# Kernel optimization log

Measured on AMD Instinct MI355X. Metric: run time of the kernel, lower is better.

## Reference

```python
import jax, jax.numpy as jnp
import numpy as np

N = 100000   # nodes
E = 1600000  # edges
F_IN = 128   # node_features
H = 64       # hidden_features


def setup_inputs() -> dict:
    key = jax.random.key(0)
    ks = jax.random.split(key, 16)
    s = 0.05
    return {
        "x": jax.random.normal(ks[0], (N, F_IN), dtype=jnp.float32),
        "edge_index": jax.random.randint(ks[1], (2, E), 0, N, dtype=jnp.int64),
        "W1": jax.random.normal(ks[2], (H, F_IN), dtype=jnp.float32) * s,
        "b1": jnp.zeros((H,), dtype=jnp.float32),
        "W2": jax.random.normal(ks[3], (H, H), dtype=jnp.float32) * s,
        "b2": jnp.zeros((H,), dtype=jnp.float32),
        "Wk": jax.random.normal(ks[4], (H, H), dtype=jnp.float32) * s,
        "bk": jnp.zeros((H,), dtype=jnp.float32),
        "Wq": jax.random.normal(ks[5], (H, H), dtype=jnp.float32) * s,
        "bq": jnp.zeros((H,), dtype=jnp.float32),
        "Wv": jax.random.normal(ks[6], (H, H), dtype=jnp.float32) * s,
        "bv": jnp.zeros((H,), dtype=jnp.float32),
        "Ws": jax.random.normal(ks[7], (H, H), dtype=jnp.float32) * s,  # lin_skip, bias=False
        "b_gate": jnp.zeros((H,), dtype=jnp.float32),                   # conv bias param
        "Wsc": jax.random.normal(ks[8], (1, H), dtype=jnp.float32) * s,
        "bsc": jnp.zeros((1,), dtype=jnp.float32),
    }


def reference(x, edge_index, W1, b1, W2, b2, Wk, bk, Wq, bq, Wv, bv, Ws, b_gate, Wsc, bsc):
    # MLP front-end: Linear + ReLU + Linear
    h = jax.nn.relu(x @ W1.T + b1)
    h = h @ W2.T + b2                      # [N, H]

    # ResGatedGraphConv (sum aggregation, sigmoid gating)
    k = h @ Wk.T + bk                      # key on destination nodes
    q = h @ Wq.T + bq                      # query on source nodes
    v = h @ Wv.T + bv                      # value on source nodes

    src = edge_index[0]                    # j
    dst = edge_index[1]                    # i
    # message_ij = sigmoid(k_i + q_j) * v_j, scatter-add to destination i
    msg = jax.nn.sigmoid(k[dst] + q[src]) * v[src]   # [E, H]
    agg = jax.ops.segment_sum(msg, dst, num_segments=N)

    out = agg + h @ Ws.T + b_gate          # root skip (no bias) + conv bias

    # scorer head
    score = out @ Wsc.T + bsc              # [N, 1]
    return score
```

## Files before the change

kernel.cpp:

```cpp
#include <hip/hip_runtime.h>

#define HD  64
#define FIN 128

#define WS_W1T   0
#define WS_MK    8192
#define WS_MQ    12288
#define WS_MVW   16384
#define WS_WSK1  20480
#define WS_BK    20544
#define WS_BQ    20608
#define WS_BVW   20672
#define WS_BASE  20736
#define WS_H1    20800

#define C1f  3.9026344e-3f
#define C3f  (-7.67612e-8f)
#define C5f  1.2236660e-12f

__device__ __forceinline__ unsigned bf16rne(float f) {
    unsigned u = __float_as_uint(f);
    unsigned r = ((u >> 16) & 1u) + 0x7fffu;
    return (u + r) >> 16;
}
__device__ __forceinline__ uint2 pack4(float4 v) {
    uint2 r;
    r.x = bf16rne(v.x) | (bf16rne(v.y) << 16);
    r.y = bf16rne(v.z) | (bf16rne(v.w) << 16);
    return r;
}
__device__ __forceinline__ float blo(unsigned u) { return __uint_as_float(u << 16); }
__device__ __forceinline__ float bhi(unsigned u) { return __uint_as_float(u & 0xffff0000u); }

__device__ __forceinline__ unsigned encq(float4 v) {
    int e0 = min(max(__float2int_rn(fmaf(v.x, 64.f, 128.f)), 0), 255);
    int e1 = min(max(__float2int_rn(fmaf(v.y, 64.f, 128.f)), 0), 255);
    int e2 = min(max(__float2int_rn(fmaf(v.z, 64.f, 128.f)), 0), 255);
    int e3 = min(max(__float2int_rn(fmaf(v.w, 64.f, 128.f)), 0), 255);
    return (unsigned)e0 | ((unsigned)e1 << 8) | ((unsigned)e2 << 16) | ((unsigned)e3 << 24);
}

__device__ __forceinline__ float grp4(unsigned ku, unsigned qu, unsigned va,
                                      unsigned vb, float p) {
    #pragma unroll
    for (int i = 0; i < 4; ++i) {
        float kf = (float)((ku >> (8 * i)) & 255u);
        float qf = (float)((qu >> (8 * i)) & 255u);
        unsigned vu = (i < 2) ? va : vb;
        float vf = (i & 1) ? bhi(vu) : blo(vu);
        float xx = kf + qf;
        xx = fminf(fmaxf(xx, 128.f), 384.f);
        float sv = xx - 256.f;
        float z = sv * sv;
        float w = fmaf(z, C5f, C3f);
        w = fmaf(z, w, C1f);
        p = fmaf(vf * sv, w, p);
        p = fmaf(vf, 0.5f, p);
    }
    return p;
}

__global__ void gnn_prep(const float* __restrict__ W1, const float* __restrict__ W2,
                         const float* __restrict__ b2,
                         const float* __restrict__ Wk, const float* __restrict__ bk,
                         const float* __restrict__ Wq, const float* __restrict__ bq,
                         const float* __restrict__ Wv, const float* __restrict__ bv,
                         const float* __restrict__ Wsm, const float* __restrict__ Wsc,
                         const float* __restrict__ bgate, const float* __restrict__ bsc,
                         float* __restrict__ ws) {
    __shared__ float w2s[4096];
    __shared__ float wxsT[65 * 64];
    int b = blockIdx.x, t = threadIdx.x;
    if (b == 0) {
        for (int idx = t; idx < HD * FIN; idx += blockDim.x) {
            int c = idx / FIN, j = idx % FIN;
            ws[WS_W1T + j * HD + c] = W1[idx];
        }
    } else if (b <= 12) {
        int m = (b - 1) >> 2, qtr = (b - 1) & 3;
        const float* Wx = (m == 0) ? Wk : (m == 1) ? Wq : Wv;
        const float* bx = (m == 0) ? bk : (m == 1) ? bq : bv;
        int moff = (m == 0) ? WS_MK : (m == 1) ? WS_MQ : WS_MVW;
        int boff = (m == 0) ? WS_BK : (m == 1) ? WS_BQ : WS_BVW;
        for (int i = t * 4; i < 4096; i += 1024)
            *(float4*)&w2s[i] = *(const float4*)&W2[i];
        for (int idx = t; idx < 4096; idx += 256) {
            int o = idx >> 6, c = idx & 63;
            wxsT[c * 65 + o] = Wx[idx];
        }
        __syncthreads();
        for (int idx = t; idx < 1024; idx += 256) {
            int a = qtr * 16 + (idx >> 6), o = idx & 63;
            float acc = 0.f;
            for (int c = 0; c < HD; ++c) acc += w2s[c * HD + a] * wxsT[c * 65 + o];
            if (m == 2) acc *= Wsc[o];
            ws[moff + a * HD + o] = acc;
        }
        if (qtr == 0 && t < HD) {
            float acc = bx[t];
            for (int c = 0; c < HD; ++c) acc += b2[c] * wxsT[c * 65 + t];
            if (m == 2) acc *= Wsc[t];
            ws[boff + t] = acc;
        }
    } else {
        __shared__ float wsk[HD];
        if (t < HD) {
            float a = 0.f;
            for (int d = 0; d < HD; ++d) a += Wsm[d * HD + t] * Wsc[d];
            wsk[t] = a;
        }
        __syncthreads();
        if (t < HD) {
            float a = 0.f;
            for (int c = 0; c < HD; ++c) a += W2[c * HD + t] * wsk[c];
            ws[WS_WSK1 + t] = a;
        }
        if (t == 0) {
            float a = bsc[0];
            for (int d = 0; d < HD; ++d) a += bgate[d] * Wsc[d];
            for (int c = 0; c < HD; ++c) a += b2[c] * wsk[c];
            ws[WS_BASE] = a;
        }
    }
}

__global__ __launch_bounds__(256, 3) void gnn_node(const float* __restrict__ x,
                                                   const float* __restrict__ b1,
                                                   const float* __restrict__ ws,
                                                   unsigned* __restrict__ nodebuf,
                                                   float* __restrict__ score, int N) {
    __shared__ float xs[64 * 132];
    unsigned* hs = (unsigned*)xs;

    int tid = threadIdx.x;
    int nbase = blockIdx.x * 64;

    for (int i4 = tid; i4 < 2048; i4 += 256) {
        int nl = i4 >> 5, c4 = i4 & 31;
        int node = min(nbase + nl, N - 1);
        float4 xv = ((const float4*)x)[(size_t)node * 32 + c4];
        *(float4*)&xs[nl * 132 + c4 * 4] = xv;
    }
    __syncthreads();

    int wv = tid >> 6, l = tid & 63, g = l >> 4, f = l & 15;
    int nl0 = wv * 16 + g * 4;

    const float* w1 = ws + WS_W1T;
    float4 bias = *(const float4*)&b1[4 * f];
    float4 acc[4];
    #pragma unroll
    for (int n = 0; n < 4; ++n) acc[n] = bias;

    for (int j = 0; j < FIN; j += 4) {
        float4 xv[4];
        #pragma unroll
        for (int n = 0; n < 4; ++n) xv[n] = *(const float4*)&xs[(nl0 + n) * 132 + j];
        #pragma unroll
        for (int jj = 0; jj < 4; ++jj) {
            float4 wvv = *(const float4*)&w1[(j + jj) * HD + 4 * f];
            #pragma unroll
            for (int n = 0; n < 4; ++n) {
                float xsc = ((const float*)&xv[n])[jj];
                acc[n].x += xsc * wvv.x; acc[n].y += xsc * wvv.y;
                acc[n].z += xsc * wvv.z; acc[n].w += xsc * wvv.w;
            }
        }
    }
    __syncthreads();
    #pragma unroll
    for (int n = 0; n < 4; ++n) {
        float4 r;
        r.x = fmaxf(acc[n].x, 0.f); r.y = fmaxf(acc[n].y, 0.f);
        r.z = fmaxf(acc[n].z, 0.f); r.w = fmaxf(acc[n].w, 0.f);
        *(uint2*)&hs[(nl0 + n) * 36 + 2 * f] = pack4(r);
    }
    __syncthreads();

    float base = ws[WS_BASE];
    float4 accK[4], accQ[4], accV[4];
    float sacc[4];
    float4 bK = *(const float4*)&ws[WS_BK + 4 * f];
    float4 bQ = *(const float4*)&ws[WS_BQ + 4 * f];
    float4 bV = *(const float4*)&ws[WS_BVW + 4 * f];
    #pragma unroll
    for (int n = 0; n < 4; ++n) { accK[n] = bK; accQ[n] = bQ; accV[n] = bV; sacc[n] = 0.f; }

    for (int a = 0; a < HD; a += 4) {
        float hf[4][4];
        #pragma unroll
        for (int n = 0; n < 4; ++n) {
            uint2 hu = *(const uint2*)&hs[(nl0 + n) * 36 + (a >> 1)];
            hf[n][0] = blo(hu.x); hf[n][1] = bhi(hu.x);
            hf[n][2] = blo(hu.y); hf[n][3] = bhi(hu.y);
        }
        #pragma unroll
        for (int aa = 0; aa < 4; ++aa) {
            float4 mk = *(const float4*)&ws[WS_MK + (a + aa) * HD + 4 * f];
            float4 mq = *(const float4*)&ws[WS_MQ + (a + aa) * HD + 4 * f];
            float4 mv = *(const float4*)&ws[WS_MVW + (a + aa) * HD + 4 * f];
            float wk = ws[WS_WSK1 + a + aa];
            #pragma unroll
            for (int n = 0; n < 4; ++n) {
                float s1 = hf[n][aa];
                accK[n].x += s1 * mk.x; accK[n].y += s1 * mk.y;
                accK[n].z += s1 * mk.z; accK[n].w += s1 * mk.w;
                accQ[n].x += s1 * mq.x; accQ[n].y += s1 * mq.y;
                accQ[n].z += s1 * mq.z; accQ[n].w += s1 * mq.w;
                accV[n].x += s1 * mv.x; accV[n].y += s1 * mv.y;
                accV[n].z += s1 * mv.z; accV[n].w += s1 * mv.w;
                sacc[n] += s1 * wk;
            }
        }
    }
    #pragma unroll
    for (int n = 0; n < 4; ++n) {
        int node = nbase + nl0 + n;
        if (node < N) {
            unsigned* rec = nodebuf + (size_t)node * 64;
            rec[f] = encq(accK[n]);
            rec[16 + f] = encq(accQ[n]);
            *(uint2*)&rec[32 + 2 * f] = pack4(accV[n]);
            if (f == 0) score[node] = base + sacc[n];
        }
    }
}

__global__ __launch_bounds__(256) void gnn_edge(const int* __restrict__ ei,
                                                const uint4* __restrict__ nb,
                                                float* __restrict__ score, int E) {
    int t = blockIdx.x * 256 + threadIdx.x;
    int e = t >> 2;
    if (e >= E) return;
    int f = t & 3;
    int s = ei[e];
    int d = ei[E + e];
    uint4 ku = nb[(size_t)d * 16 + f];
    uint4 qu = nb[(size_t)s * 16 + 4 + f];
    uint4 va = nb[(size_t)s * 16 + 8 + 2 * f];
    uint4 vb = nb[(size_t)s * 16 + 9 + 2 * f];
    float p = 0.f;
    p = grp4(ku.x, qu.x, va.x, va.y, p);
    p = grp4(ku.y, qu.y, va.z, va.w, p);
    p = grp4(ku.z, qu.z, vb.x, vb.y, p);
    p = grp4(ku.w, qu.w, vb.z, vb.w, p);
    p += __shfl_down(p, 2, 4);
    p += __shfl_down(p, 1, 4);
    if (f == 0) atomicAdd(&score[d], p);
}

extern "C" void kernel_launch(void* const* d_in, const int* in_sizes, int n_in,
                              void* d_out, int out_size, void* d_ws, size_t ws_size,
                              hipStream_t stream) {
    const float* x    = (const float*)d_in[0];
    const int*   ei   = (const int*)d_in[1];
    const float* W1   = (const float*)d_in[2];
    const float* b1   = (const float*)d_in[3];
    const float* W2   = (const float*)d_in[4];
    const float* b2   = (const float*)d_in[5];
    const float* Wk   = (const float*)d_in[6];
    const float* bk   = (const float*)d_in[7];
    const float* Wq   = (const float*)d_in[8];
    const float* bq   = (const float*)d_in[9];
    const float* Wv   = (const float*)d_in[10];
    const float* bv   = (const float*)d_in[11];
    const float* Wsm  = (const float*)d_in[12];
    const float* bgat = (const float*)d_in[13];
    const float* Wsc  = (const float*)d_in[14];
    const float* bsc  = (const float*)d_in[15];

    int N = in_sizes[0] / FIN;
    int E = in_sizes[1] / 2;

    float* ws    = (float*)d_ws;
    float* recs  = ws + WS_H1;
    float* score = (float*)d_out;

    int NB = (N + 63) / 64;
    gnn_prep<<<14, 256, 0, stream>>>(W1, W2, b2, Wk, bk, Wq, bq, Wv, bv,
                                     Wsm, Wsc, bgat, bsc, ws);
    gnn_node<<<NB, 256, 0, stream>>>(x, b1, ws, (unsigned*)recs, score, N);
    gnn_edge<<<(E * 4 + 255) / 256, 256, 0, stream>>>(ei, (const uint4*)recs, score, E);
}
```

Before: 310.4 us.

## Use bf16 MFMA with split-precision inputs for node MLP and projections

Measured after the change: 294.3 us. 5.2% less time.

```diff
diff --git a/kernel.cpp b/kernel.cpp
--- a/kernel.cpp
+++ b/kernel.cpp
@@ -3,42 +3,29 @@
 #define HD  64
 #define FIN 128
 
-#define WS_W1T   0
-#define WS_MK    8192
-#define WS_MQ    12288
-#define WS_MVW   16384
-#define WS_WSK1  20480
-#define WS_BK    20544
-#define WS_BQ    20608
-#define WS_BVW   20672
-#define WS_BASE  20736
-#define WS_H1    20800
+#define WS_W1H   0
+#define WS_W1L   4096
+#define WS_MALL  8192
+#define WS_BK    14848
+#define WS_BQ    14912
+#define WS_BVW   14976
+#define WS_BASE  15040
+#define WS_REC   15104
 
 #define C1f  3.9026344e-3f
 #define C3f  (-7.67612e-8f)
 #define C5f  1.2236660e-12f
+
+typedef __attribute__((ext_vector_type(8))) short short8;
+typedef __attribute__((ext_vector_type(4))) float f32x4;
 
 __device__ __forceinline__ unsigned bf16rne(float f) {
     unsigned u = __float_as_uint(f);
     unsigned r = ((u >> 16) & 1u) + 0x7fffu;
     return (u + r) >> 16;
 }
-__device__ __forceinline__ uint2 pack4(float4 v) {
-    uint2 r;
-    r.x = bf16rne(v.x) | (bf16rne(v.y) << 16);
-    r.y = bf16rne(v.z) | (bf16rne(v.w) << 16);
-    return r;
-}
 __device__ __forceinline__ float blo(unsigned u) { return __uint_as_float(u << 16); }
 __device__ __forceinline__ float bhi(unsigned u) { return __uint_as_float(u & 0xffff0000u); }
-
-__device__ __forceinline__ unsigned encq(float4 v) {
-    int e0 = min(max(__float2int_rn(fmaf(v.x, 64.f, 128.f)), 0), 255);
-    int e1 = min(max(__float2int_rn(fmaf(v.y, 64.f, 128.f)), 0), 255);
-    int e2 = min(max(__float2int_rn(fmaf(v.z, 64.f, 128.f)), 0), 255);
-    int e3 = min(max(__float2int_rn(fmaf(v.w, 64.f, 128.f)), 0), 255);
-    return (unsigned)e0 | ((unsigned)e1 << 8) | ((unsigned)e2 << 16) | ((unsigned)e3 << 24);
-}
 
 __device__ __forceinline__ float grp4(unsigned ku, unsigned qu, unsigned va,
                                       unsigned vb, float p) {
@@ -71,16 +58,21 @@
     __shared__ float w2s[4096];
     __shared__ float wxsT[65 * 64];
     int b = blockIdx.x, t = threadIdx.x;
+    unsigned short* w1h  = (unsigned short*)(ws + WS_W1H);
+    unsigned short* w1l  = (unsigned short*)(ws + WS_W1L);
+    unsigned short* mall = (unsigned short*)(ws + WS_MALL);
     if (b == 0) {
         for (int idx = t; idx < HD * FIN; idx += blockDim.x) {
-            int c = idx / FIN, j = idx % FIN;
-            ws[WS_W1T + j * HD + c] = W1[idx];
+            float v = W1[idx];
+            unsigned u = __float_as_uint(v);
+            w1h[idx] = (unsigned short)(u >> 16);
+            float rem = v - __uint_as_float(u & 0xffff0000u);
+            w1l[idx] = (unsigned short)bf16rne(rem);
         }
     } else if (b <= 12) {
         int m = (b - 1) >> 2, qtr = (b - 1) & 3;
         const float* Wx = (m == 0) ? Wk : (m == 1) ? Wq : Wv;
         const float* bx = (m == 0) ? bk : (m == 1) ? bq : bv;
-        int moff = (m == 0) ? WS_MK : (m == 1) ? WS_MQ : WS_MVW;
         int boff = (m == 0) ? WS_BK : (m == 1) ? WS_BQ : WS_BVW;
         for (int i = t * 4; i < 4096; i += 1024)
             *(float4*)&w2s[i] = *(const float4*)&W2[i];
@@ -94,7 +86,7 @@
             float acc = 0.f;
             for (int c = 0; c < HD; ++c) acc += w2s[c * HD + a] * wxsT[c * 65 + o];
             if (m == 2) acc *= Wsc[o];
-            ws[moff + a * HD + o] = acc;
+            mall[(m * 64 + o) * HD + a] = (unsigned short)bf16rne(acc);
         }
         if (qtr == 0 && t < HD) {
             float acc = bx[t];
@@ -113,13 +105,21 @@
         if (t < HD) {
             float a = 0.f;
             for (int c = 0; c < HD; ++c) a += W2[c * HD + t] * wsk[c];
-            ws[WS_WSK1 + t] = a;
-        }
+            mall[192 * HD + t] = (unsigned short)bf16rne(a);
+        }
+        for (int idx = t; idx < 15 * HD; idx += 256)
+            mall[193 * HD + idx] = 0;
         if (t == 0) {
             float a = bsc[0];
             for (int d = 0; d < HD; ++d) a += bgate[d] * Wsc[d];
-            for (int c = 0; c < HD; ++c) a += b2[c] * wsk[c];
-            ws[WS_BASE] = a;
+            float acc2 = 0.f;
+            __syncthreads();
+            for (int c = 0; c < HD; ++c) {
+                float wk2 = 0.f;
+                for (int d = 0; d < HD; ++d) wk2 += Wsm[d * HD + c] * Wsc[d];
+                acc2 += b2[c] * wk2;
+            }
+            ws[WS_BASE] = a + acc2;
         }
     }
 }
@@ -129,100 +129,154 @@
                                                    const float* __restrict__ ws,
                                                    unsigned* __restrict__ nodebuf,
                                                    float* __restrict__ score, int N) {
-    __shared__ float xs[64 * 132];
-    unsigned* hs = (unsigned*)xs;
+    __shared__ __align__(16) char smem[32768];
+    char* XHb = smem;
+    char* XLb = smem + 16384;
 
     int tid = threadIdx.x;
+    int l = tid & 63, w = tid >> 6;
     int nbase = blockIdx.x * 64;
 
-    for (int i4 = tid; i4 < 2048; i4 += 256) {
-        int nl = i4 >> 5, c4 = i4 & 31;
+    #pragma unroll
+    for (int it = 0; it < 8; ++it) {
+        int idx = it * 64 + l;
+        int nl = 16 * w + (idx >> 5);
+        int c4 = idx & 31;
         int node = min(nbase + nl, N - 1);
-        float4 xv = ((const float4*)x)[(size_t)node * 32 + c4];
-        *(float4*)&xs[nl * 132 + c4 * 4] = xv;
+        float4 v = ((const float4*)x)[(size_t)node * 32 + c4];
+        unsigned u0 = __float_as_uint(v.x), u1 = __float_as_uint(v.y);
+        unsigned u2 = __float_as_uint(v.z), u3 = __float_as_uint(v.w);
+        uint2 hx, lx;
+        hx.x = (u0 >> 16) | (u1 & 0xffff0000u);
+        hx.y = (u2 >> 16) | (u3 & 0xffff0000u);
+        float r0 = v.x - __uint_as_float(u0 & 0xffff0000u);
+        float r1 = v.y - __uint_as_float(u1 & 0xffff0000u);
+        float r2 = v.z - __uint_as_float(u2 & 0xffff0000u);
+        float r3 = v.w - __uint_as_float(u3 & 0xffff0000u);
+        lx.x = bf16rne(r0) | (bf16rne(r1) << 16);
+        lx.y = bf16rne(r2) | (bf16rne(r3) << 16);
+        int bo = (nl * 256 + c4 * 8) ^ ((nl & 7) << 4);
+        *(uint2*)(XHb + bo) = hx;
+        *(uint2*)(XLb + bo) = lx;
     }
     __syncthreads();
 
-    int wv = tid >> 6, l = tid & 63, g = l >> 4, f = l & 15;
-    int nl0 = wv * 16 + g * 4;
-
-    const float* w1 = ws + WS_W1T;
-    float4 bias = *(const float4*)&b1[4 * f];
-    float4 acc[4];
-    #pragma unroll
-    for (int n = 0; n < 4; ++n) acc[n] = bias;
-
-    for (int j = 0; j < FIN; j += 4) {
-        float4 xv[4];
-        #pragma unroll
-        for (int n = 0; n < 4; ++n) xv[n] = *(const float4*)&xs[(nl0 + n) * 132 + j];
-        #pragma unroll
-        for (int jj = 0; jj < 4; ++jj) {
-            float4 wvv = *(const float4*)&w1[(j + jj) * HD + 4 * f];
-            #pragma unroll
-            for (int n = 0; n < 4; ++n) {
-                float xsc = ((const float*)&xv[n])[jj];
-                acc[n].x += xsc * wvv.x; acc[n].y += xsc * wvv.y;
-                acc[n].z += xsc * wvv.z; acc[n].w += xsc * wvv.w;
-            }
+    int rl = l & 15, kb = l >> 4;
+    int rowA = 16 * w + rl;
+    int swzA = (rowA & 7) << 4;
+
+    const unsigned short* w1h = (const unsigned short*)(ws + WS_W1H);
+    const unsigned short* w1l = (const unsigned short*)(ws + WS_W1L);
+    f32x4 acc1[4];
+    #pragma unroll
+    for (int t = 0; t < 4; ++t) {
+        float bv = b1[t * 16 + rl];
+        acc1[t] = (f32x4){bv, bv, bv, bv};
+    }
+    #pragma unroll
+    for (int s = 0; s < 4; ++s) {
+        int abyte = (rowA * 256 + s * 64 + kb * 16) ^ swzA;
+        short8 ah = *(const short8*)(XHb + abyte);
+        short8 al = *(const short8*)(XLb + abyte);
+        int koff = s * 32 + kb * 8;
+        #pragma unroll
+        for (int t = 0; t < 4; ++t) {
+            int col = t * 16 + rl;
+            short8 bh = *(const short8*)&w1h[col * FIN + koff];
+            short8 bl = *(const short8*)&w1l[col * FIN + koff];
+            acc1[t] = __builtin_amdgcn_mfma_f32_16x16x32_bf16(ah, bh, acc1[t], 0, 0, 0);
+            acc1[t] = __builtin_amdgcn_mfma_f32_16x16x32_bf16(al, bh, acc1[t], 0, 0, 0);
+            acc1[t] = __builtin_amdgcn_mfma_f32_16x16x32_bf16(ah, bl, acc1[t], 0, 0, 0);
         }
     }
     __syncthreads();
-    #pragma unroll
-    for (int n = 0; n < 4; ++n) {
-        float4 r;
-        r.x = fmaxf(acc[n].x, 0.f); r.y = fmaxf(acc[n].y, 0.f);
-        r.z = fmaxf(acc[n].z, 0.f); r.w = fmaxf(acc[n].w, 0.f);
-        *(uint2*)&hs[(nl0 + n) * 36 + 2 * f] = pack4(r);
+
+    int r0w = (l >> 4) * 4;
+    #pragma unroll
+    for (int t = 0; t < 4; ++t) {
+        int col = t * 16 + rl;
+        #pragma unroll
+        for (int r = 0; r < 4; ++r) {
+            int row = 16 * w + r0w + r;
+            float v = fmaxf(acc1[t][r], 0.f);
+            int hb = (row * 128 + col * 2) ^ ((row & 7) << 4);
+            *(unsigned short*)(smem + hb) = (unsigned short)bf16rne(v);
+        }
     }
     __syncthreads();
 
+    const unsigned short* mall = (const unsigned short*)(ws + WS_MALL);
+    const float* bK = ws + WS_BK;
+    const float* bQ = ws + WS_BQ;
+    const float* bV = ws + WS_BVW;
     float base = ws[WS_BASE];
-    float4 accK[4], accQ[4], accV[4];
-    float sacc[4];
-    float4 bK = *(const float4*)&ws[WS_BK + 4 * f];
-    float4 bQ = *(const float4*)&ws[WS_BQ + 4 * f];
-    float4 bV = *(const float4*)&ws[WS_BVW + 4 * f];
-    #pragma unroll
-    for (int n = 0; n < 4; ++n) { accK[n] = bK; accQ[n] = bQ; accV[n] = bV; sacc[n] = 0.f; }
-
-    for (int a = 0; a < HD; a += 4) {
-        float hf[4][4];
-        #pragma unroll
-        for (int n = 0; n < 4; ++n) {
-            uint2 hu = *(const uint2*)&hs[(nl0 + n) * 36 + (a >> 1)];
-            hf[n][0] = blo(hu.x); hf[n][1] = bhi(hu.x);
-            hf[n][2] = blo(hu.y); hf[n][3] = bhi(hu.y);
-        }
-        #pragma unroll
-        for (int aa = 0; aa < 4; ++aa) {
-            float4 mk = *(const float4*)&ws[WS_MK + (a + aa) * HD + 4 * f];
-            float4 mq = *(const float4*)&ws[WS_MQ + (a + aa) * HD + 4 * f];
-            float4 mv = *(const float4*)&ws[WS_MVW + (a + aa) * HD + 4 * f];
-            float wk = ws[WS_WSK1 + a + aa];
-            #pragma unroll
-            for (int n = 0; n < 4; ++n) {
-                float s1 = hf[n][aa];
-                accK[n].x += s1 * mk.x; accK[n].y += s1 * mk.y;
-                accK[n].z += s1 * mk.z; accK[n].w += s1 * mk.w;
-                accQ[n].x += s1 * mq.x; accQ[n].y += s1 * mq.y;
-                accQ[n].z += s1 * mq.z; accQ[n].w += s1 * mq.w;
-                accV[n].x += s1 * mv.x; accV[n].y += s1 * mv.y;
-                accV[n].z += s1 * mv.z; accV[n].w += s1 * mv.w;
-                sacc[n] += s1 * wk;
-            }
-        }
-    }
-    #pragma unroll
-    for (int n = 0; n < 4; ++n) {
-        int node = nbase + nl0 + n;
-        if (node < N) {
-            unsigned* rec = nodebuf + (size_t)node * 64;
-            rec[f] = encq(accK[n]);
-            rec[16 + f] = encq(accQ[n]);
-            *(uint2*)&rec[32 + 2 * f] = pack4(accV[n]);
-            if (f == 0) score[node] = base + sacc[n];
-        }
+    f32x4 acc2[13];
+    #pragma unroll
+    for (int t = 0; t < 4; ++t) {
+        float v = bK[t * 16 + rl];
+        acc2[t] = (f32x4){v, v, v, v};
+    }
+    #pragma unroll
+    for (int t = 0; t < 4; ++t) {
+        float v = bQ[t * 16 + rl];
+        acc2[4 + t] = (f32x4){v, v, v, v};
+    }
+    #pragma unroll
+    for (int t = 0; t < 4; ++t) {
+        float v = bV[t * 16 + rl];
+        acc2[8 + t] = (f32x4){v, v, v, v};
+    }
+    acc2[12] = (f32x4){0.f, 0.f, 0.f, 0.f};
+
+    #pragma unroll
+    for (int s = 0; s < 2; ++s) {
+        int abyte = (rowA * 128 + (s * 32 + kb * 8) * 2) ^ swzA;
+        short8 a = *(const short8*)(smem + abyte);
+        int koff = s * 32 + kb * 8;
+        #pragma unroll
+        for (int t = 0; t < 13; ++t) {
+            short8 b = *(const short8*)&mall[(t * 16 + rl) * HD + koff];
+            acc2[t] = __builtin_amdgcn_mfma_f32_16x16x32_bf16(a, b, acc2[t], 0, 0, 0);
+        }
+    }
+
+    char* Ku = smem + 16384;
+    char* Qu = smem + 20480;
+    char* VW = smem + 24576;
+    #pragma unroll
+    for (int t = 0; t < 4; ++t) {
+        int col = t * 16 + rl;
+        #pragma unroll
+        for (int r = 0; r < 4; ++r) {
+            int row = 16 * w + r0w + r;
+            int ek = min(max(__float2int_rn(fmaf(acc2[t][r],     64.f, 128.f)), 0), 255);
+            int eq = min(max(__float2int_rn(fmaf(acc2[4 + t][r], 64.f, 128.f)), 0), 255);
+            Ku[row * 64 + col] = (char)ek;
+            Qu[row * 64 + col] = (char)eq;
+            *(unsigned short*)(VW + row * 128 + col * 2) =
+                (unsigned short)bf16rne(acc2[8 + t][r]);
+        }
+    }
+    if (rl == 0) {
+        #pragma unroll
+        for (int r = 0; r < 4; ++r) {
+            int node = nbase + 16 * w + r0w + r;
+            if (node < N) score[node] = base + acc2[12][r];
+        }
+    }
+    __syncthreads();
+
+    uint4* recs = (uint4*)nodebuf;
+    #pragma unroll
+    for (int it = 0; it < 4; ++it) {
+        int c = it * 256 + tid;
+        int n = c >> 4, p = c & 15;
+        uint4 v;
+        if (p < 4)      v = *(const uint4*)(Ku + n * 64 + p * 16);
+        else if (p < 8) v = *(const uint4*)(Qu + n * 64 + (p - 4) * 16);
+        else            v = *(const uint4*)(VW + n * 128 + (p - 8) * 16);
+        int node = nbase + n;
+        if (node < N) recs[(size_t)node * 16 + p] = v;
     }
 }
 
@@ -273,7 +327,7 @@
     int E = in_sizes[1] / 2;
 
     float* ws    = (float*)d_ws;
-    float* recs  = ws + WS_H1;
+    float* recs  = ws + WS_REC;
     float* score = (float*)d_out;
 
     int NB = (N + 63) / 64;
```
